# Kernel tuning notes

Hardware: AMD Instinct MI355X
Metric: run time of the kernel (lower is better)

## Reference

```python
import jax, jax.numpy as jnp
import numpy as np

N = 8192          # mesh vertices
E = 49152         # directed edges (avg degree 6)
M = 25            # kernel_size per pseudo-dim
DIM = 3           # pseudo-coordinate dim
K = M ** DIM      # 15625 weight matrices per layer
S = 2 ** DIM      # 8 nonzero degree-1 B-spline products per edge
LC, UC = -0.22703196, 0.36853024   # curvature range
LM, UM = 1.2585511, 1.648841       # myelin range
R = 10.0
LAYER_DIMS = [(2, 32), (32, 64), (64, 64), (64, 32), (32, 1)]


def transform(x):
    # rescale curv/myelin channels into [-R, R] with clamping (matches torch masking)
    t0 = (x[:, 0] - LC) / (UC - LC) * (2.0 * R) - R
    t1 = (x[:, 1] - LM) / (UM - LM) * (2.0 * R) - R
    return jnp.stack([jnp.clip(t0, -R, R), jnp.clip(t1, -R, R)], axis=1)


def spline_basis(pseudo):
    # open B-spline, degree 1: v in [0, M-1); 8 corner products per edge
    v = pseudo * (M - 1)
    lo = jnp.floor(v)
    f = v - lo                                                    # [E, DIM]
    lo = lo.astype(jnp.int32)
    bits = (jnp.arange(S)[:, None] >> jnp.arange(DIM)[None, :]) & 1   # [S, DIM]
    oh = bits.astype(pseudo.dtype)
    basis = jnp.prod(oh[None] * f[:, None, :] + (1.0 - oh[None]) * (1.0 - f[:, None, :]), axis=-1)  # [E, S]
    strides = (M ** jnp.arange(DIM)).astype(jnp.int32)
    wi = jnp.sum((lo[:, None, :] + bits[None]) * strides[None, None, :], axis=-1)  # [E, S] kernel indices
    return basis, wi


def spline_conv(h, src, dst, basis, wi, W, root, bias):
    xj = h[src]                                             # [E, Fin] gather
    msg = jnp.zeros((xj.shape[0], W.shape[2]), h.dtype)
    for s in range(S):                                      # fixed 8-way basis loop
        msg = msg + basis[:, s, None] * jnp.einsum('ei,eio->eo', xj, W[wi[:, s]])
    agg = jax.ops.segment_sum(msg, dst, num_segments=N)     # scatter-sum (norm=False)
    return agg + h @ root + bias


def setup_inputs() -> dict:
    key = jax.random.key(0)
    ks = jax.random.split(key, 3 + 2 * len(LAYER_DIMS))
    inp = {
        "x": jax.random.normal(ks[0], (N, 2), dtype=jnp.float32),
        "edge_index": jax.random.randint(ks[1], (2, E), 0, N),
        "pseudo": jax.random.uniform(ks[2], (E, DIM), dtype=jnp.float32),
    }
    for i, (fi, fo) in enumerate(LAYER_DIMS):
        kw, kr = ks[3 + 2 * i], ks[4 + 2 * i]
        inp[f"W{i+1}"] = jax.random.normal(kw, (K, fi, fo), dtype=jnp.float32) / np.float32(np.sqrt(fi * S))
        inp[f"root{i+1}"] = jax.random.normal(kr, (fi, fo), dtype=jnp.float32) / np.float32(np.sqrt(fi))
        inp[f"b{i+1}"] = jnp.zeros((fo,), dtype=jnp.float32)
    return inp


def reference(x, edge_index, pseudo, W1, root1, b1, W2, root2, b2, W3, root3, b3,
              W4, root4, b4, W5, root5, b5):
    src, dst = edge_index[0], edge_index[1]
    basis, wi = spline_basis(pseudo)   # shared across all 5 layers, as in the torch model
    h = transform(x)
    for W, r, b in ((W1, root1, b1), (W2, root2, b2), (W3, root3, b3),
                    (W4, root4, b4), (W5, root5, b5)):
        h = jax.nn.elu(spline_conv(h, src, dst, basis, wi, W, r, b))
    return h.reshape(-1)
```

## Files before the change

### kernel.cpp

```cpp
#include <hip/hip_runtime.h>
#include <math.h>

#define NV 8192
#define EV 49152
#define KK 15625

typedef __attribute__((ext_vector_type(8))) short bf16x8;
typedef __attribute__((ext_vector_type(4))) float f32x4;

__device__ __forceinline__ void atomAddF(float* p, float v) {
    unsafeAtomicAdd(p, v);
}

__device__ __forceinline__ unsigned short bf16rne(float x) {
    unsigned u = __float_as_uint(x);
    unsigned r = u + 0x7FFFu + ((u >> 16) & 1u);
    return (unsigned short)(r >> 16);
}
__device__ __forceinline__ float bf16tof(unsigned short h) {
    return __uint_as_float(((unsigned)h) << 16);
}

__device__ __forceinline__ void edge_frac(const float* __restrict__ pseudo, int e,
                                          float f[3], int lo[3]) {
#pragma unroll
    for (int j = 0; j < 3; ++j) {
        float v = pseudo[e * 3 + j] * 24.0f;
        float fl = floorf(v);
        int l = (int)fl;
        l = l < 0 ? 0 : (l > 23 ? 23 : l);
        lo[j] = l;
        f[j] = v - (float)l;
    }
}

__global__ void prep_kernel(const float* __restrict__ x, float* __restrict__ h0,
                            int* __restrict__ counts, float* __restrict__ agg) {
    int gt = blockIdx.x * blockDim.x + threadIdx.x;
    if (gt < NV) {
        const float LC = -0.22703196f, UC = 0.36853024f;
        const float LM = 1.2585511f, UM = 1.648841f;
        const float R = 10.0f;
        float t0 = (x[gt * 2 + 0] - LC) / (UC - LC) * (2.0f * R) - R;
        float t1 = (x[gt * 2 + 1] - LM) / (UM - LM) * (2.0f * R) - R;
        h0[gt * 2 + 0] = fminf(fmaxf(t0, -R), R);
        h0[gt * 2 + 1] = fminf(fmaxf(t1, -R), R);
    }
    if (gt < KK) counts[gt] = 0;
    if (gt < NV * 64) agg[gt] = 0.0f;
}

__global__ void hist_kernel(const float* __restrict__ pseudo, int* __restrict__ counts) {
    int e = blockIdx.x * blockDim.x + threadIdx.x;
    if (e >= EV) return;
    float f[3]; int lo[3];
    edge_frac(pseudo, e, f, lo);
#pragma unroll
    for (int s = 0; s < 8; ++s) {
        int wi = (lo[0] + (s & 1)) + 25 * (lo[1] + ((s >> 1) & 1)) + 625 * (lo[2] + ((s >> 2) & 1));
        atomicAdd(&counts[wi], 1);
    }
}

__global__ void scan_kernel(const int* __restrict__ counts, int* __restrict__ offsets,
                            int* __restrict__ cursor) {
    __shared__ int sums[256];
    const int CH = 62;
    int t = threadIdx.x;
    int base = t * CH;
    int s = 0;
    for (int i = 0; i < CH; ++i) {
        int idx = base + i;
        if (idx < KK) s += counts[idx];
    }
    sums[t] = s;
    __syncthreads();
    for (int d = 1; d < 256; d <<= 1) {
        int v = (t >= d) ? sums[t - d] : 0;
        __syncthreads();
        sums[t] += v;
        __syncthreads();
    }
    int run = (t > 0) ? sums[t - 1] : 0;
    for (int i = 0; i < CH; ++i) {
        int idx = base + i;
        if (idx < KK) {
            offsets[idx] = run;
            cursor[idx] = run;
            run += counts[idx];
        }
    }
    if (t == 255) offsets[KK] = run;
}

__global__ void scatter_kernel(const float* __restrict__ pseudo, const int* __restrict__ ei,
                               int* __restrict__ cursor,
                               int2* __restrict__ pair_sb, int* __restrict__ pair_dst) {
    int e = blockIdx.x * blockDim.x + threadIdx.x;
    if (e >= EV) return;
    float f[3]; int lo[3];
    edge_frac(pseudo, e, f, lo);
    int src = ei[e];
    int dst = ei[EV + e];
#pragma unroll
    for (int s = 0; s < 8; ++s) {
        float b = ((s & 1) ? f[0] : 1.0f - f[0]) *
                  (((s >> 1) & 1) ? f[1] : 1.0f - f[1]) *
                  (((s >> 2) & 1) ? f[2] : 1.0f - f[2]);
        int wi = (lo[0] + (s & 1)) + 25 * (lo[1] + ((s >> 1) & 1)) + 625 * (lo[2] + ((s >> 2) & 1));
        int pos = atomicAdd(&cursor[wi], 1);
        pair_sb[pos] = make_int2(src, __float_as_int(b));
        pair_dst[pos] = dst;
    }
}

template <int FIN, int FOUT>
__global__ __launch_bounds__(256) void conv_v7(
    const float* __restrict__ h, const float* __restrict__ W,
    const int* __restrict__ offsets, const int2* __restrict__ pair_sb,
    const int* __restrict__ pair_dst, float* __restrict__ agg) {
    constexpr int KT = FIN / 32;
    constexpr int NT = FOUT / 16;
    const int J = KK * NT;
    int w = threadIdx.x >> 6;
    int lane = threadIdx.x & 63;
    int l15 = lane & 15;
    int lg = lane >> 4;
    int nwaves = gridDim.x * 4;

    for (int job = blockIdx.x * 4 + w; job < J; job += nwaves) {
        int k = job / NT;
        int nslice = job % NT;
        int start = offsets[k];
        int n = offsets[k + 1] - start;
        if (n <= 0) continue;

        const float* Wk = W + (size_t)k * (FIN * FOUT) + nslice * 16 + l15;
        bf16x8 Bh[KT], Bl[KT];
#pragma unroll
        for (int k0 = 0; k0 < KT; ++k0)
#pragma unroll
            for (int i = 0; i < 8; ++i) {
                float wv = Wk[(size_t)(k0 * 32 + lg * 8 + i) * FOUT];
                unsigned short hi = bf16rne(wv);
                unsigned short lo = bf16rne(wv - bf16tof(hi));
                Bh[k0][i] = (short)hi;
                Bl[k0][i] = (short)lo;
            }

        const int2* psb = pair_sb + start;
        const int* pdst = pair_dst + start;

        for (int m0 = 0; m0 < n; m0 += 16) {
            int ra = m0 + l15;
            bool va = ra < n;
            int2 sb = psb[va ? ra : 0];
            float b = va ? __int_as_float(sb.y) : 0.0f;
            const float* xr = h + (size_t)sb.x * FIN + lg * 8;

            f32x4 acc = (f32x4){0.f, 0.f, 0.f, 0.f};
#pragma unroll
            for (int k0 = 0; k0 < KT; ++k0) {
                float4 v0 = *(const float4*)(xr + k0 * 32);
                float4 v1 = *(const float4*)(xr + k0 * 32 + 4);
                float xv[8] = {v0.x * b, v0.y * b, v0.z * b, v0.w * b,
                               v1.x * b, v1.y * b, v1.z * b, v1.w * b};
                bf16x8 Ah, Al;
#pragma unroll
                for (int i = 0; i < 8; ++i) {
                    unsigned short hi = bf16rne(xv[i]);
                    unsigned short lo = bf16rne(xv[i] - bf16tof(hi));
                    Ah[i] = (short)hi;
                    Al[i] = (short)lo;
                }
                acc = __builtin_amdgcn_mfma_f32_16x16x32_bf16(Ah, Bh[k0], acc, 0, 0, 0);
                acc = __builtin_amdgcn_mfma_f32_16x16x32_bf16(Ah, Bl[k0], acc, 0, 0, 0);
                acc = __builtin_amdgcn_mfma_f32_16x16x32_bf16(Al, Bh[k0], acc, 0, 0, 0);
            }

#pragma unroll
            for (int j = 0; j < 4; ++j) {
                int rm = m0 + lg * 4 + j;
                if (rm < n) {
                    int d = pdst[rm];
                    atomAddF(&agg[(size_t)d * FOUT + nslice * 16 + l15], acc[j]);
                }
            }
        }
    }
}

__global__ __launch_bounds__(256) void conv_l1(
    const float* __restrict__ h, const float* __restrict__ W,
    const int* __restrict__ offsets, const int2* __restrict__ pair_sb,
    const int* __restrict__ pair_dst, float* __restrict__ agg) {
    int w = threadIdx.x >> 6;
    int lane = threadIdx.x & 63;
    int o = lane & 31;
    int g = lane >> 5;
    int nwaves = gridDim.x * 4;
    const float2* h2 = (const float2*)h;
    for (int k = blockIdx.x * 4 + w; k < KK; k += nwaves) {
        int start = offsets[k];
        int n = offsets[k + 1] - start;
        if (n <= 0) continue;
        const float* Wk = W + (size_t)k * 64;
        float w0 = Wk[o], w1 = Wk[32 + o];
        for (int r = g; r < n; r += 2) {
            int2 sb = pair_sb[start + r];
            float b = __int_as_float(sb.y);
            int dst = pair_dst[start + r];
            float2 xv = h2[sb.x];
            atomAddF(&agg[(size_t)dst * 32 + o], b * (xv.x * w0 + xv.y * w1));
        }
    }
}

__global__ __launch_bounds__(256) void conv_f1(
    const float* __restrict__ h, const float* __restrict__ W,
    const int* __restrict__ offsets, const int2* __restrict__ pair_sb,
    const int* __restrict__ pair_dst, float* __restrict__ agg) {
    int w = threadIdx.x >> 6;
    int lane = threadIdx.x & 63;
    int i = lane & 31;
    int g = lane >> 5;
    int nwaves = gridDim.x * 4;
    for (int k = blockIdx.x * 4 + w; k < KK; k += nwaves) {
        int start = offsets[k];
        int n = offsets[k + 1] - start;
        if (n <= 0) continue;
        float wk = W[(size_t)k * 32 + i];
        for (int r = g; r < n; r += 2) {
            int2 sb = pair_sb[start + r];
            float b = __int_as_float(sb.y);
            int dst = pair_dst[start + r];
            float val = h[(size_t)sb.x * 32 + i] * wk * b;
#pragma unroll
            for (int d = 16; d >= 1; d >>= 1) val += __shfl_xor(val, d, 32);
            if (i == 0) atomAddF(&agg[dst], val);
        }
    }
}

template <int FIN, int FOUT>
__global__ void node_kernel(const float* __restrict__ h, float* __restrict__ agg,
                            const float* __restrict__ root, const float* __restrict__ bias,
                            float* __restrict__ hout) {
    int idx = blockIdx.x * blockDim.x + threadIdx.x;
    if (idx >= NV * 64) return;
    if (idx < NV * FOUT) {
        int n = idx / FOUT, o = idx % FOUT;
        float acc = agg[idx] + bias[o];
#pragma unroll
        for (int i = 0; i < FIN; ++i) acc += h[n * FIN + i] * root[i * FOUT + o];
        hout[idx] = acc > 0.0f ? acc : expm1f(acc);
    }
    agg[idx] = 0.0f;
}

extern "C" void kernel_launch(void* const* d_in, const int* in_sizes, int n_in,
                              void* d_out, int out_size, void* d_ws, size_t ws_size,
                              hipStream_t stream) {
    const float* x      = (const float*)d_in[0];
    const int*   ei     = (const int*)d_in[1];
    const float* pseudo = (const float*)d_in[2];
    const float* W1 = (const float*)d_in[3];
    const float* r1 = (const float*)d_in[4];
    const float* b1 = (const float*)d_in[5];
    const float* W2 = (const float*)d_in[6];
    const float* r2 = (const float*)d_in[7];
    const float* b2 = (const float*)d_in[8];
    const float* W3 = (const float*)d_in[9];
    const float* r3 = (const float*)d_in[10];
    const float* b3 = (const float*)d_in[11];
    const float* W4 = (const float*)d_in[12];
    const float* r4 = (const float*)d_in[13];
    const float* b4 = (const float*)d_in[14];
    const float* W5 = (const float*)d_in[15];
    const float* r5 = (const float*)d_in[16];
    const float* b5 = (const float*)d_in[17];

    char* ws = (char*)d_ws;
    size_t off = 0;
    auto alloc = [&](size_t bytes) {
        void* p = ws + off;
        off += (bytes + 255) & ~(size_t)255;
        return p;
    };
    int*   counts   = (int*)alloc(KK * sizeof(int));
    int*   offsets  = (int*)alloc((KK + 1) * sizeof(int));
    int*   cursor   = (int*)alloc(KK * sizeof(int));
    int2*  pair_sb  = (int2*)alloc((size_t)EV * 8 * sizeof(int2));
    int*   pair_dst = (int*)alloc((size_t)EV * 8 * sizeof(int));
    float* hA       = (float*)alloc((size_t)NV * 64 * sizeof(float));
    float* hB       = (float*)alloc((size_t)NV * 64 * sizeof(float));
    float* agg      = (float*)alloc((size_t)NV * 64 * sizeof(float));

    const int NGRID = (NV * 64 + 255) / 256;
    const int CGRID = 2048;

    prep_kernel<<<NGRID, 256, 0, stream>>>(x, hA, counts, agg);
    hist_kernel<<<(EV + 255) / 256, 256, 0, stream>>>(pseudo, counts);
    scan_kernel<<<1, 256, 0, stream>>>(counts, offsets, cursor);
    scatter_kernel<<<(EV + 255) / 256, 256, 0, stream>>>(pseudo, ei, cursor, pair_sb, pair_dst);

    conv_l1<<<CGRID, 256, 0, stream>>>(hA, W1, offsets, pair_sb, pair_dst, agg);
    node_kernel<2, 32><<<NGRID, 256, 0, stream>>>(hA, agg, r1, b1, hB);

    conv_v7<32, 64><<<CGRID, 256, 0, stream>>>(hB, W2, offsets, pair_sb, pair_dst, agg);
    node_kernel<32, 64><<<NGRID, 256, 0, stream>>>(hB, agg, r2, b2, hA);

    conv_v7<64, 64><<<CGRID, 256, 0, stream>>>(hA, W3, offsets, pair_sb, pair_dst, agg);
    node_kernel<64, 64><<<NGRID, 256, 0, stream>>>(hA, agg, r3, b3, hB);

    conv_v7<64, 32><<<CGRID, 256, 0, stream>>>(hB, W4, offsets, pair_sb, pair_dst, agg);
    node_kernel<64, 32><<<NGRID, 256, 0, stream>>>(hB, agg, r4, b4, hA);

    conv_f1<<<CGRID, 256, 0, stream>>>(hA, W5, offsets, pair_sb, pair_dst, agg);
    node_kernel<32, 1><<<NGRID, 256, 0, stream>>>(hA, agg, r5, b5, (float*)d_out);
}
```

Measured before the change: 551.5 us.

## Store activations as pre-split bf16 hi/lo pairs and apply basis after MFMA

After: 551.1 us. Within noise of the previous version (-0.1%).

```diff
diff --git a/kernel.cpp b/kernel.cpp
--- a/kernel.cpp
+++ b/kernel.cpp
@@ -95,7 +95,7 @@
 
 __global__ void scatter_kernel(const float* __restrict__ pseudo, const int* __restrict__ ei,
                                int* __restrict__ cursor,
-                               int2* __restrict__ pair_sb, int* __restrict__ pair_dst) {
+                               int* __restrict__ pair_src, int2* __restrict__ pair_db) {
     int e = blockIdx.x * blockDim.x + threadIdx.x;
     if (e >= EV) return;
     float f[3]; int lo[3];
@@ -109,16 +109,17 @@
                   (((s >> 2) & 1) ? f[2] : 1.0f - f[2]);
         int wi = (lo[0] + (s & 1)) + 25 * (lo[1] + ((s >> 1) & 1)) + 625 * (lo[2] + ((s >> 2) & 1));
         int pos = atomicAdd(&cursor[wi], 1);
-        pair_sb[pos] = make_int2(src, __float_as_int(b));
-        pair_dst[pos] = dst;
+        pair_src[pos] = src;
+        pair_db[pos] = make_int2(dst, __float_as_int(b));
     }
 }
 
 template <int FIN, int FOUT>
-__global__ __launch_bounds__(256) void conv_v7(
-    const float* __restrict__ h, const float* __restrict__ W,
-    const int* __restrict__ offsets, const int2* __restrict__ pair_sb,
-    const int* __restrict__ pair_dst, float* __restrict__ agg) {
+__global__ __launch_bounds__(256) void conv_v8(
+    const unsigned short* __restrict__ hhi, const unsigned short* __restrict__ hlo,
+    const float* __restrict__ W,
+    const int* __restrict__ offsets, const int* __restrict__ pair_src,
+    const int2* __restrict__ pair_db, float* __restrict__ agg) {
     constexpr int KT = FIN / 32;
     constexpr int NT = FOUT / 16;
     const int J = KK * NT;
@@ -130,7 +131,7 @@
 
     for (int job = blockIdx.x * 4 + w; job < J; job += nwaves) {
         int k = job / NT;
-        int nslice = job % NT;
+        int nslice = job - k * NT;
         int start = offsets[k];
         int n = offsets[k + 1] - start;
         if (n <= 0) continue;
@@ -148,31 +149,20 @@
                 Bl[k0][i] = (short)lo;
             }
 
-        const int2* psb = pair_sb + start;
-        const int* pdst = pair_dst + start;
+        const int* psrc = pair_src + start;
+        const int2* pdb = pair_db + start;
 
         for (int m0 = 0; m0 < n; m0 += 16) {
             int ra = m0 + l15;
-            bool va = ra < n;
-            int2 sb = psb[va ? ra : 0];
-            float b = va ? __int_as_float(sb.y) : 0.0f;
-            const float* xr = h + (size_t)sb.x * FIN + lg * 8;
+            int src = psrc[ra < n ? ra : 0];
+            const unsigned short* rhi = hhi + (size_t)src * FIN + lg * 8;
+            const unsigned short* rlo = hlo + (size_t)src * FIN + lg * 8;
 
             f32x4 acc = (f32x4){0.f, 0.f, 0.f, 0.f};
 #pragma unroll
             for (int k0 = 0; k0 < KT; ++k0) {
-                float4 v0 = *(const float4*)(xr + k0 * 32);
-                float4 v1 = *(const float4*)(xr + k0 * 32 + 4);
-                float xv[8] = {v0.x * b, v0.y * b, v0.z * b, v0.w * b,
-                               v1.x * b, v1.y * b, v1.z * b, v1.w * b};
-                bf16x8 Ah, Al;
-#pragma unroll
-                for (int i = 0; i < 8; ++i) {
-                    unsigned short hi = bf16rne(xv[i]);
-                    unsigned short lo = bf16rne(xv[i] - bf16tof(hi));
-                    Ah[i] = (short)hi;
-                    Al[i] = (short)lo;
-                }
+                bf16x8 Ah = *(const bf16x8*)(rhi + k0 * 32);
+                bf16x8 Al = *(const bf16x8*)(rlo + k0 * 32);
                 acc = __builtin_amdgcn_mfma_f32_16x16x32_bf16(Ah, Bh[k0], acc, 0, 0, 0);
                 acc = __builtin_amdgcn_mfma_f32_16x16x32_bf16(Ah, Bl[k0], acc, 0, 0, 0);
                 acc = __builtin_amdgcn_mfma_f32_16x16x32_bf16(Al, Bh[k0], acc, 0, 0, 0);
@@ -182,8 +172,9 @@
             for (int j = 0; j < 4; ++j) {
                 int rm = m0 + lg * 4 + j;
                 if (rm < n) {
-                    int d = pdst[rm];
-                    atomAddF(&agg[(size_t)d * FOUT + nslice * 16 + l15], acc[j]);
+                    int2 db = pdb[rm];
+                    atomAddF(&agg[(size_t)db.x * FOUT + nslice * 16 + l15],
+                             acc[j] * __int_as_float(db.y));
                 }
             }
         }
@@ -192,8 +183,8 @@
 
 __global__ __launch_bounds__(256) void conv_l1(
     const float* __restrict__ h, const float* __restrict__ W,
-    const int* __restrict__ offsets, const int2* __restrict__ pair_sb,
-    const int* __restrict__ pair_dst, float* __restrict__ agg) {
+    const int* __restrict__ offsets, const int* __restrict__ pair_src,
+    const int2* __restrict__ pair_db, float* __restrict__ agg) {
     int w = threadIdx.x >> 6;
     int lane = threadIdx.x & 63;
     int o = lane & 31;
@@ -207,19 +198,20 @@
         const float* Wk = W + (size_t)k * 64;
         float w0 = Wk[o], w1 = Wk[32 + o];
         for (int r = g; r < n; r += 2) {
-            int2 sb = pair_sb[start + r];
-            float b = __int_as_float(sb.y);
-            int dst = pair_dst[start + r];
-            float2 xv = h2[sb.x];
-            atomAddF(&agg[(size_t)dst * 32 + o], b * (xv.x * w0 + xv.y * w1));
+            int src = pair_src[start + r];
+            int2 db = pair_db[start + r];
+            float b = __int_as_float(db.y);
+            float2 xv = h2[src];
+            atomAddF(&agg[(size_t)db.x * 32 + o], b * (xv.x * w0 + xv.y * w1));
         }
     }
 }
 
 __global__ __launch_bounds__(256) void conv_f1(
-    const float* __restrict__ h, const float* __restrict__ W,
-    const int* __restrict__ offsets, const int2* __restrict__ pair_sb,
-    const int* __restrict__ pair_dst, float* __restrict__ agg) {
+    const unsigned short* __restrict__ hhi, const unsigned short* __restrict__ hlo,
+    const float* __restrict__ W,
+    const int* __restrict__ offsets, const int* __restrict__ pair_src,
+    const int2* __restrict__ pair_db, float* __restrict__ agg) {
     int w = threadIdx.x >> 6;
     int lane = threadIdx.x & 63;
     int i = lane & 31;
@@ -231,31 +223,70 @@
         if (n <= 0) continue;
         float wk = W[(size_t)k * 32 + i];
         for (int r = g; r < n; r += 2) {
-            int2 sb = pair_sb[start + r];
-            float b = __int_as_float(sb.y);
-            int dst = pair_dst[start + r];
-            float val = h[(size_t)sb.x * 32 + i] * wk * b;
+            int src = pair_src[start + r];
+            int2 db = pair_db[start + r];
+            float b = __int_as_float(db.y);
+            float hv = bf16tof(hhi[(size_t)src * 32 + i]) + bf16tof(hlo[(size_t)src * 32 + i]);
+            float val = hv * wk * b;
 #pragma unroll
             for (int d = 16; d >= 1; d >>= 1) val += __shfl_xor(val, d, 32);
-            if (i == 0) atomAddF(&agg[dst], val);
-        }
-    }
+            if (i == 0) atomAddF(&agg[db.x], val);
+        }
+    }
+}
+
+__global__ void node1_kernel(const float* __restrict__ h, float* __restrict__ agg,
+                             const float* __restrict__ root, const float* __restrict__ bias,
+                             unsigned short* __restrict__ ohi, unsigned short* __restrict__ olo) {
+    int idx = blockIdx.x * blockDim.x + threadIdx.x;
+    if (idx >= NV * 64) return;
+    if (idx < NV * 32) {
+        int n = idx >> 5, o = idx & 31;
+        float acc = agg[idx] + bias[o] + h[n * 2] * root[o] + h[n * 2 + 1] * root[32 + o];
+        float v = acc > 0.0f ? acc : expm1f(acc);
+        unsigned short hi = bf16rne(v);
+        ohi[idx] = hi;
+        olo[idx] = bf16rne(v - bf16tof(hi));
+    }
+    agg[idx] = 0.0f;
 }
 
 template <int FIN, int FOUT>
-__global__ void node_kernel(const float* __restrict__ h, float* __restrict__ agg,
-                            const float* __restrict__ root, const float* __restrict__ bias,
-                            float* __restrict__ hout) {
+__global__ void node_p(const unsigned short* __restrict__ hhi,
+                       const unsigned short* __restrict__ hlo, float* __restrict__ agg,
+                       const float* __restrict__ root, const float* __restrict__ bias,
+                       unsigned short* __restrict__ ohi, unsigned short* __restrict__ olo) {
     int idx = blockIdx.x * blockDim.x + threadIdx.x;
     if (idx >= NV * 64) return;
     if (idx < NV * FOUT) {
         int n = idx / FOUT, o = idx % FOUT;
         float acc = agg[idx] + bias[o];
 #pragma unroll
-        for (int i = 0; i < FIN; ++i) acc += h[n * FIN + i] * root[i * FOUT + o];
-        hout[idx] = acc > 0.0f ? acc : expm1f(acc);
+        for (int i = 0; i < FIN; ++i) {
+            float hv = bf16tof(hhi[(size_t)n * FIN + i]) + bf16tof(hlo[(size_t)n * FIN + i]);
+            acc += hv * root[i * FOUT + o];
+        }
+        float v = acc > 0.0f ? acc : expm1f(acc);
+        unsigned short hi = bf16rne(v);
+        ohi[idx] = hi;
+        olo[idx] = bf16rne(v - bf16tof(hi));
     }
     agg[idx] = 0.0f;
+}
+
+__global__ void node5_kernel(const unsigned short* __restrict__ hhi,
+                             const unsigned short* __restrict__ hlo,
+                             const float* __restrict__ agg, const float* __restrict__ root,
+                             const float* __restrict__ bias, float* __restrict__ out) {
+    int n = blockIdx.x * blockDim.x + threadIdx.x;
+    if (n >= NV) return;
+    float acc = agg[n] + bias[0];
+#pragma unroll
+    for (int i = 0; i < 32; ++i) {
+        float hv = bf16tof(hhi[(size_t)n * 32 + i]) + bf16tof(hlo[(size_t)n * 32 + i]);
+        acc += hv * root[i];
+    }
+    out[n] = acc > 0.0f ? acc : expm1f(acc);
 }
 
 extern "C" void kernel_launch(void* const* d_in, const int* in_sizes, int n_in,
@@ -290,32 +321,35 @@
     int*   counts   = (int*)alloc(KK * sizeof(int));
     int*   offsets  = (int*)alloc((KK + 1) * sizeof(int));
     int*   cursor   = (int*)alloc(KK * sizeof(int));
-    int2*  pair_sb  = (int2*)alloc((size_t)EV * 8 * sizeof(int2));
-    int*   pair_dst = (int*)alloc((size_t)EV * 8 * sizeof(int));
-    float* hA       = (float*)alloc((size_t)NV * 64 * sizeof(float));
-    float* hB       = (float*)alloc((size_t)NV * 64 * sizeof(float));
+    int*   pair_src = (int*)alloc((size_t)EV * 8 * sizeof(int));
+    int2*  pair_db  = (int2*)alloc((size_t)EV * 8 * sizeof(int2));
+    float* h0       = (float*)alloc((size_t)NV * 2 * sizeof(float));
+    unsigned short* pAhi = (unsigned short*)alloc((size_t)NV * 64 * sizeof(unsigned short));
+    unsigned short* pAlo = (unsigned short*)alloc((size_t)NV * 64 * sizeof(unsigned short));
+    unsigned short* pBhi = (unsigned short*)alloc((size_t)NV * 64 * sizeof(unsigned short));
+    unsigned short* pBlo = (unsigned short*)alloc((size_t)NV * 64 * sizeof(unsigned short));
     float* agg      = (float*)alloc((size_t)NV * 64 * sizeof(float));
 
     const int NGRID = (NV * 64 + 255) / 256;
     const int CGRID = 2048;
 
-    prep_kernel<<<NGRID, 256, 0, stream>>>(x, hA, counts, agg);
+    prep_kernel<<<NGRID, 256, 0, stream>>>(x, h0, counts, agg);
     hist_kernel<<<(EV + 255) / 256, 256, 0, stream>>>(pseudo, counts);
     scan_kernel<<<1, 256, 0, stream>>>(counts, offsets, cursor);
-    scatter_kernel<<<(EV + 255) / 256, 256, 0, stream>>>(pseudo, ei, cursor, pair_sb, pair_dst);
-
-    conv_l1<<<CGRID, 256, 0, stream>>>(hA, W1, offsets, pair_sb, pair_dst, agg);
-    node_kernel<2, 32><<<NGRID, 256, 0, stream>>>(hA, agg, r1, b1, hB);
-
-    conv_v7<32, 64><<<CGRID, 256, 0, stream>>>(hB, W2, offsets, pair_sb, pair_dst, agg);
-    node_kernel<32, 64><<<NGRID, 256, 0, stream>>>(hB, agg, r2, b2, hA);
-
-    conv_v7<64, 64><<<CGRID, 256, 0, stream>>>(hA, W3, offsets, pair_sb, pair_dst, agg);
-    node_kernel<64, 64><<<NGRID, 256, 0, stream>>>(hA, agg, r3, b3, hB);
-
-    conv_v7<64, 32><<<CGRID, 256, 0, stream>>>(hB, W4, offsets, pair_sb, pair_dst, agg);
-    node_kernel<64, 32><<<NGRID, 256, 0, stream>>>(hB, agg, r4, b4, hA);
-
-    conv_f1<<<CGRID, 256, 0, stream>>>(hA, W5, offsets, pair_sb, pair_dst, agg);
-    node_kernel<32, 1><<<NGRID, 256, 0, stream>>>(hA, agg, r5, b5, (float*)d_out);
-}
+    scatter_kernel<<<(EV + 255) / 256, 256, 0, stream>>>(pseudo, ei, cursor, pair_src, pair_db);
+
+    conv_l1<<<CGRID, 256, 0, stream>>>(h0, W1, offsets, pair_src, pair_db, agg);
+    node1_kernel<<<NGRID, 256, 0, stream>>>(h0, agg, r1, b1, pAhi, pAlo);
+
+    conv_v8<32, 64><<<CGRID, 256, 0, stream>>>(pAhi, pAlo, W2, offsets, pair_src, pair_db, agg);
+    node_p<32, 64><<<NGRID, 256, 0, stream>>>(pAhi, pAlo, agg, r2, b2, pBhi, pBlo);
+
+    conv_v8<64, 64><<<CGRID, 256, 0, stream>>>(pBhi, pBlo, W3, offsets, pair_src, pair_db, agg);
+    node_p<64, 64><<<NGRID, 256, 0, stream>>>(pBhi, pBlo, agg, r3, b3, pAhi, pAlo);
+
+    conv_v8<64, 32><<<CGRID, 256, 0, stream>>>(pAhi, pAlo, W4, offsets, pair_src, pair_db, agg);
+    node_p<64, 32><<<NGRID, 256, 0, stream>>>(pAhi, pAlo, agg, r4, b4, pBhi, pBlo);
+
+    conv_f1<<<CGRID, 256, 0, stream>>>(pBhi, pBlo, W5, offsets, pair_src, pair_db, agg);
+    node5_kernel<<<(NV + 255) / 256, 256, 0, stream>>>(pBhi, pBlo, agg, r5, b5, (float*)d_out);
+}
```
